# Kernel tuning notes

Hardware: AMD Instinct MI355X
Metric: run time of the kernel (lower is better)

The kernel has to match this reference:

```python
import jax, jax.numpy as jnp
import numpy as np

B, D, N = 131072, 512, 101
BIG = 1e9
NORM_EPS = 0.1  # F.normalize eps


def setup_inputs() -> dict:
    key = jax.random.key(0)
    k1, k2, k3 = jax.random.split(key, 3)
    embeddings = jax.random.normal(k1, (B, D), dtype=jnp.float32)
    centers_weight = jax.random.normal(k2, (N, D), dtype=jnp.float32)
    labels = jax.random.randint(k3, (B,), 0, N, dtype=jnp.int64)
    return {"embeddings": embeddings, "centers_weight": centers_weight, "labels": labels}


def reference(embeddings, centers_weight, labels):
    # ---- center (MSE) term: per-sample squared distance to own center ----
    gathered = centers_weight[labels]                     # [B, D]
    center_loss = ((embeddings - gathered) ** 2).sum(axis=1)  # [B] (reduction=None)

    # ---- margin term (original operates on .data -> detached) ----
    W = jax.lax.stop_gradient(centers_weight)
    norms = jnp.sqrt((W * W).sum(axis=1, keepdims=True))
    C = W / jnp.maximum(norms, NORM_EPS)                  # F.normalize(p=2, eps=0.1)
    n = C.shape[0]
    dist = 1.0 - C @ C.T                                  # [N, N] cosine distance
    idx = jnp.arange(n)
    diff = jnp.abs(idx[:, None] - idx[None, :])
    dist = dist + BIG * (diff == 0)                       # mask diagonal (eye)

    # neighbor distances BEFORE they are masked out
    d_lower = jnp.diagonal(dist, offset=-1)               # Dist[i, i-1], i = 1..n-1
    d_upper = jnp.diagonal(dist, offset=1)                # Dist[i, i+1], i = 0..n-2

    dist_masked = dist + BIG * (diff == 1)                # mask adjacent centers
    min_dist = dist_masked.min(axis=1)                    # Dist[i, NegIdx]

    margin = (jax.nn.relu(2.0 * d_lower - min_dist[1:]).sum()
              + jax.nn.relu(2.0 * d_upper - min_dist[:-1]).sum()) / n

    return margin + center_loss.mean()
```

## Files before the change

### kernel.cpp

```cpp
#include <hip/hip_runtime.h>

#define BB 131072
#define DD 512
#define NN 101
#define D4 (DD / 4)
#define TOT (BB * D4)
#define CBLK 2048
#define GBLK 256
#define NPAIR (NN * NN)

__global__ __launch_bounds__(256) void fused_kernel(
    const float4* __restrict__ emb, const float4* __restrict__ ctr,
    const int* __restrict__ labels,
    float* __restrict__ partial,
    float* __restrict__ G)
{
    int b = blockIdx.x;
    if (b < CBLK) {
        int tid    = b * 256 + threadIdx.x;
        int stride = CBLK * 256;
        float local = 0.f;
        for (int i = tid; i < TOT; i += stride) {
            int s   = i >> 7;
            int d4  = i & (D4 - 1);
            int lab = labels[s];
            float4 e = emb[i];
            float4 c = ctr[lab * D4 + d4];
            float dx = e.x - c.x;
            float dy = e.y - c.y;
            float dz = e.z - c.z;
            float dw = e.w - c.w;
            local += dx * dx + dy * dy + dz * dz + dw * dw;
        }
        for (int off = 32; off > 0; off >>= 1)
            local += __shfl_down(local, off);
        __shared__ float wsum[4];
        int lane = threadIdx.x & 63;
        int wid  = threadIdx.x >> 6;
        if (lane == 0) wsum[wid] = local;
        __syncthreads();
        if (threadIdx.x == 0)
            partial[b] = wsum[0] + wsum[1] + wsum[2] + wsum[3];
    } else {
        int wv   = (b - CBLK) * 4 + (threadIdx.x >> 6);
        int lane = threadIdx.x & 63;
        for (int p = wv; p < NPAIR; p += GBLK * 4) {
            int i = p / NN;
            int j = p % NN;
            const float4* wi = ctr + i * D4;
            const float4* wj = ctr + j * D4;
            float dot = 0.f;
#pragma unroll
            for (int r = 0; r < 2; r++) {
                int d4 = lane + r * 64;
                float4 a = wi[d4];
                float4 c = wj[d4];
                dot += a.x * c.x + a.y * c.y + a.z * c.z + a.w * c.w;
            }
            for (int off = 32; off > 0; off >>= 1)
                dot += __shfl_down(dot, off);
            if (lane == 0) G[p] = dot;
        }
    }
}

__global__ __launch_bounds__(256) void finalize_kernel(
    const float* __restrict__ G, const float* __restrict__ partial,
    float* __restrict__ out)
{
    int t = threadIdx.x;

    double dsum = 0.0;
    for (int i = t; i < CBLK; i += 256)
        dsum += (double)partial[i];
    for (int off = 32; off > 0; off >>= 1)
        dsum += __shfl_down(dsum, off);
    __shared__ double dacc[4];
    if ((t & 63) == 0) dacc[t >> 6] = dsum;

    __shared__ float denom[NN];
    __shared__ float mind[NN];
    if (t < NN)
        denom[t] = fmaxf(sqrtf(G[t * NN + t]), 0.1f);
    __syncthreads();
    if (t < NN) {
        float di = denom[t];
        float mn = 1e30f;
        for (int j = 0; j < NN; j++) {
            if (j >= t - 1 && j <= t + 1) continue;
            float d = 1.0f - G[t * NN + j] / (di * denom[j]);
            mn = fminf(mn, d);
        }
        mind[t] = mn;
    }
    __syncthreads();
    float contrib = 0.f;
    if (t >= 1 && t < NN) {
        float dl = 1.0f - G[t * NN + (t - 1)] / (denom[t] * denom[t - 1]);
        contrib += fmaxf(2.0f * dl - mind[t], 0.0f);
    }
    if (t < NN - 1) {
        float du = 1.0f - G[t * NN + (t + 1)] / (denom[t] * denom[t + 1]);
        contrib += fmaxf(2.0f * du - mind[t], 0.0f);
    }
    for (int off = 32; off > 0; off >>= 1)
        contrib += __shfl_down(contrib, off);
    __shared__ float wsum2[4];
    if ((t & 63) == 0) wsum2[t >> 6] = contrib;
    __syncthreads();
    if (t == 0) {
        float margin = (wsum2[0] + wsum2[1] + wsum2[2] + wsum2[3]) / (float)NN;
        double center = (dacc[0] + dacc[1] + dacc[2] + dacc[3]) / (double)BB;
        out[0] = margin + (float)center;
    }
}

extern "C" void kernel_launch(void* const* d_in, const int* in_sizes, int n_in,
                              void* d_out, int out_size, void* d_ws, size_t ws_size,
                              hipStream_t stream) {
    const float* emb    = (const float*)d_in[0];
    const float* ctr    = (const float*)d_in[1];
    const int*   labels = (const int*)d_in[2];
    float* out = (float*)d_out;

    float* partial = (float*)d_ws;
    float* G       = (float*)((char*)d_ws + CBLK * 4);

    fused_kernel<<<CBLK + GBLK, 256, 0, stream>>>(
        (const float4*)emb, (const float4*)ctr, labels, partial, G);
    finalize_kernel<<<1, 256, 0, stream>>>(G, partial, out);
}
```

Baseline: 82.02 us.

## Merge Gram work into all blocks and unroll streaming loop with nontemporal loads

The separate Gram-matrix blocks are removed; every block now first computes up to three center-pair dot products with its four waves, then streams its share of the embeddings. The embedding loop runs a fixed 64 iterations, unrolled four at a time, so four label, embedding and center loads are issued before any arithmetic. Embedding loads are marked nontemporal to keep the small, heavily reused center table resident in cache. The grid is halved to 1024 blocks with a min-blocks-per-CU launch bound; the risk is fewer waves in flight per CU to hide memory latency, plus a short Gram prologue that delays every block's streaming.

```diff
diff --git a/kernel.cpp b/kernel.cpp
--- a/kernel.cpp
+++ b/kernel.cpp
@@ -3,58 +3,40 @@
 #define BB 131072
 #define DD 512
 #define NN 101
-#define D4 (DD / 4)
+#define D4 128
 #define TOT (BB * D4)
-#define CBLK 2048
-#define GBLK 256
+#define CBLK 1024
+#define STR (CBLK * 256)
+#define NITER 64
+#define NWAVE (CBLK * 4)
 #define NPAIR (NN * NN)
 
-__global__ __launch_bounds__(256) void fused_kernel(
-    const float4* __restrict__ emb, const float4* __restrict__ ctr,
+typedef float f4 __attribute__((ext_vector_type(4)));
+
+__global__ __launch_bounds__(256, 4) void fused_kernel(
+    const f4* __restrict__ emb, const f4* __restrict__ ctr,
     const int* __restrict__ labels,
     float* __restrict__ partial,
     float* __restrict__ G)
 {
-    int b = blockIdx.x;
-    if (b < CBLK) {
-        int tid    = b * 256 + threadIdx.x;
-        int stride = CBLK * 256;
-        float local = 0.f;
-        for (int i = tid; i < TOT; i += stride) {
-            int s   = i >> 7;
-            int d4  = i & (D4 - 1);
-            int lab = labels[s];
-            float4 e = emb[i];
-            float4 c = ctr[lab * D4 + d4];
-            float dx = e.x - c.x;
-            float dy = e.y - c.y;
-            float dz = e.z - c.z;
-            float dw = e.w - c.w;
-            local += dx * dx + dy * dy + dz * dz + dw * dw;
-        }
-        for (int off = 32; off > 0; off >>= 1)
-            local += __shfl_down(local, off);
-        __shared__ float wsum[4];
-        int lane = threadIdx.x & 63;
-        int wid  = threadIdx.x >> 6;
-        if (lane == 0) wsum[wid] = local;
-        __syncthreads();
-        if (threadIdx.x == 0)
-            partial[b] = wsum[0] + wsum[1] + wsum[2] + wsum[3];
-    } else {
-        int wv   = (b - CBLK) * 4 + (threadIdx.x >> 6);
-        int lane = threadIdx.x & 63;
-        for (int p = wv; p < NPAIR; p += GBLK * 4) {
+    int b    = blockIdx.x;
+    int lane = threadIdx.x & 63;
+    int wid  = threadIdx.x >> 6;
+
+    int w = b * 4 + wid;
+#pragma unroll
+    for (int rep = 0; rep < 3; rep++) {
+        int p = w + rep * NWAVE;
+        if (p < NPAIR) {
             int i = p / NN;
             int j = p % NN;
-            const float4* wi = ctr + i * D4;
-            const float4* wj = ctr + j * D4;
+            const f4* wi = ctr + i * D4;
+            const f4* wj = ctr + j * D4;
             float dot = 0.f;
 #pragma unroll
             for (int r = 0; r < 2; r++) {
-                int d4 = lane + r * 64;
-                float4 a = wi[d4];
-                float4 c = wj[d4];
+                f4 a = wi[lane + r * 64];
+                f4 c = wj[lane + r * 64];
                 dot += a.x * c.x + a.y * c.y + a.z * c.z + a.w * c.w;
             }
             for (int off = 32; off > 0; off >>= 1)
@@ -62,6 +44,44 @@
             if (lane == 0) G[p] = dot;
         }
     }
+
+    int tid = b * 256 + threadIdx.x;
+    int d4  = tid & (D4 - 1);
+    float local = 0.f;
+#pragma unroll 1
+    for (int kk = 0; kk < NITER / 4; kk++) {
+        int i0 = tid + (kk * 4 + 0) * STR;
+        int i1 = tid + (kk * 4 + 1) * STR;
+        int i2 = tid + (kk * 4 + 2) * STR;
+        int i3 = tid + (kk * 4 + 3) * STR;
+        int l0 = labels[i0 >> 7];
+        int l1 = labels[i1 >> 7];
+        int l2 = labels[i2 >> 7];
+        int l3 = labels[i3 >> 7];
+        f4 e0 = __builtin_nontemporal_load(emb + i0);
+        f4 e1 = __builtin_nontemporal_load(emb + i1);
+        f4 e2 = __builtin_nontemporal_load(emb + i2);
+        f4 e3 = __builtin_nontemporal_load(emb + i3);
+        f4 c0 = ctr[l0 * D4 + d4];
+        f4 c1 = ctr[l1 * D4 + d4];
+        f4 c2 = ctr[l2 * D4 + d4];
+        f4 c3 = ctr[l3 * D4 + d4];
+        f4 t0 = e0 - c0;
+        f4 t1 = e1 - c1;
+        f4 t2 = e2 - c2;
+        f4 t3 = e3 - c3;
+        local += t0.x * t0.x + t0.y * t0.y + t0.z * t0.z + t0.w * t0.w;
+        local += t1.x * t1.x + t1.y * t1.y + t1.z * t1.z + t1.w * t1.w;
+        local += t2.x * t2.x + t2.y * t2.y + t2.z * t2.z + t2.w * t2.w;
+        local += t3.x * t3.x + t3.y * t3.y + t3.z * t3.z + t3.w * t3.w;
+    }
+    for (int off = 32; off > 0; off >>= 1)
+        local += __shfl_down(local, off);
+    __shared__ float wsum[4];
+    if (lane == 0) wsum[wid] = local;
+    __syncthreads();
+    if (threadIdx.x == 0)
+        partial[b] = wsum[0] + wsum[1] + wsum[2] + wsum[3];
 }
 
 __global__ __launch_bounds__(256) void finalize_kernel(
@@ -126,7 +146,7 @@
     float* partial = (float*)d_ws;
     float* G       = (float*)((char*)d_ws + CBLK * 4);
 
-    fused_kernel<<<CBLK + GBLK, 256, 0, stream>>>(
-        (const float4*)emb, (const float4*)ctr, labels, partial, G);
+    fused_kernel<<<CBLK, 256, 0, stream>>>(
+        (const f4*)emb, (const f4*)ctr, labels, partial, G);
     finalize_kernel<<<1, 256, 0, stream>>>(G, partial, out);
 }
```

New measurement: 82.66 us. No clear change (+0.8%).
